# Kernel optimization log

Measured on AMD Instinct MI355X. Metric: run time of the kernel, lower is better.

Reference implementation:

```python
import jax, jax.numpy as jnp
import numpy as np
from jax import lax

SIGMAS = [0.5, 1.0, 2.0]
CHANNELS = 64

def _gaussian_kernel(sigma, channels):
    k = int(6 * sigma + 1) | 1
    x = np.arange(k, dtype=np.float32) - k // 2
    k1 = np.exp(-x ** 2 / (2 * sigma ** 2))
    k2 = np.outer(k1, k1)
    k2 = k2 / k2.sum()
    # depthwise weight layout OIHW with feature_group_count=channels: (C, 1, k, k)
    w = np.broadcast_to(k2[None, None], (channels, 1, k, k)).copy()
    return jnp.asarray(w)

_KERNELS = [_gaussian_kernel(s, CHANNELS) for s in SIGMAS]

def setup_inputs() -> dict:
    key = jax.random.key(0)
    k1, k2, k3 = jax.random.split(key, 3)
    x = jax.random.normal(k1, (8, CHANNELS, 256, 256), dtype=jnp.float32)
    fusion_w = jax.random.normal(k2, (CHANNELS, CHANNELS * len(SIGMAS)), dtype=jnp.float32) * 0.05
    fusion_b = jax.random.normal(k3, (CHANNELS,), dtype=jnp.float32) * 0.05
    return {"x": x, "fusion_w": fusion_w, "fusion_b": fusion_b}

def _depthwise(x, w):
    return lax.conv_general_dilated(
        x, w, window_strides=(1, 1), padding="SAME",
        dimension_numbers=("NCHW", "OIHW", "NCHW"),
        feature_group_count=x.shape[1])

def reference(x, fusion_w, fusion_b):
    # multi-scale depthwise Gaussian blurs, concat on channel dim
    multi_scale = jnp.concatenate([_depthwise(x, w) for w in _KERNELS], axis=1)  # [B, 3C, H, W]
    # 1x1 fusion conv + bias
    fused = jnp.einsum("bchw,oc->bohw", multi_scale, fusion_w) + fusion_b[None, :, None, None]
    return x + fused
```

## Files before the change

### kernel.cpp

```cpp
#include <hip/hip_runtime.h>
#include <hip/hip_bf16.h>
#include <math.h>

#define B_  8
#define C_  64
#define H_  256
#define W_  256
#define HW_ (H_*W_)
#define J_  192
#define TH_ 32

typedef __attribute__((ext_vector_type(8))) short short8;
typedef __attribute__((ext_vector_type(4))) float f32x4;

__device__ __forceinline__ ushort f2bf(float f) {
    union { float f; uint u; } v; v.f = f;
    uint u = v.u;
    return (ushort)((u + 0x7fffu + ((u >> 16) & 1u)) >> 16);
}
__device__ __forceinline__ float bf2f(ushort s) {
    union { uint u; float f; } v; v.u = ((uint)s) << 16;
    return v.f;
}
__device__ __forceinline__ uint pk(float a, float b) {
    return (uint)f2bf(a) | ((uint)f2bf(b) << 16);
}

__global__ __launch_bounds__(256) void k1_mix(
    const float* __restrict__ x, const float* __restrict__ fw,
    ushort* __restrict__ v)
{
    __shared__ ushort lxs[256 * 64];

    const int b      = blockIdx.x >> 8;
    const int pxbase = (blockIdx.x & 255) << 8;
    const int t      = threadIdx.x;
    const int lane   = t & 63;
    const int wv_    = t >> 6;

    {
        const int cg = lane;
        const float* xb = x + (size_t)b * C_ * HW_ + pxbase + 4 * cg;
#pragma unroll
        for (int i = 0; i < 4; ++i) {
            const int cb = wv_ * 4 + i * 16;
            const int c4 = wv_ + i * 4;
            float4 r0 = *(const float4*)(xb + (size_t)(cb + 0) * HW_);
            float4 r1 = *(const float4*)(xb + (size_t)(cb + 1) * HW_);
            float4 r2 = *(const float4*)(xb + (size_t)(cb + 2) * HW_);
            float4 r3 = *(const float4*)(xb + (size_t)(cb + 3) * HW_);
            const int sbase = c4 ^ (cg & 15);
            ushort* dst = &lxs[(4 * cg) * 64];
            *(uint2*)(dst + 0*64 + ((sbase ^ 0) * 4)) = make_uint2(pk(r0.x, r1.x), pk(r2.x, r3.x));
            *(uint2*)(dst + 1*64 + ((sbase ^ 4) * 4)) = make_uint2(pk(r0.y, r1.y), pk(r2.y, r3.y));
            *(uint2*)(dst + 2*64 + ((sbase ^ 8) * 4)) = make_uint2(pk(r0.z, r1.z), pk(r2.z, r3.z));
            *(uint2*)(dst + 3*64 + ((sbase ^ 12) * 4)) = make_uint2(pk(r0.w, r1.w), pk(r2.w, r3.w));
        }
    }

    const int n = lane & 15;
    const int q = lane >> 4;
    union Frag { short8 v; uint u[4]; };
    Frag wf[3][2];
#pragma unroll
    for (int i = 0; i < 3; ++i) {
        const int j  = (wv_ * 3 + i) * 16 + n;
        const float* wr = fw + (size_t)(j & 63) * J_ + (j >> 6) * 64;
#pragma unroll
        for (int kh = 0; kh < 2; ++kh) {
            float4 w0 = *(const float4*)(wr + kh * 32 + q * 8);
            float4 w1 = *(const float4*)(wr + kh * 32 + q * 8 + 4);
            wf[i][kh].u[0] = pk(w0.x, w0.y);
            wf[i][kh].u[1] = pk(w0.z, w0.w);
            wf[i][kh].u[2] = pk(w1.x, w1.y);
            wf[i][kh].u[3] = pk(w1.z, w1.w);
        }
    }

    __syncthreads();

    for (int mt = 0; mt < 16; ++mt) {
        const int px = mt * 16 + (lane & 15);
        const ushort* row = &lxs[px * 64];
        const int s = ((px >> 2) & 15) ^ ((px & 3) << 2);
        Frag a0, a1;
        {
            uint2 lo  = *(const uint2*)&row[((2*q    ) ^ s) * 4];
            uint2 hi  = *(const uint2*)&row[((2*q + 1) ^ s) * 4];
            a0.u[0] = lo.x;  a0.u[1] = lo.y;  a0.u[2] = hi.x;  a0.u[3] = hi.y;
            uint2 lo1 = *(const uint2*)&row[((8 + 2*q    ) ^ s) * 4];
            uint2 hi1 = *(const uint2*)&row[((8 + 2*q + 1) ^ s) * 4];
            a1.u[0] = lo1.x; a1.u[1] = lo1.y; a1.u[2] = hi1.x; a1.u[3] = hi1.y;
        }
#pragma unroll
        for (int i = 0; i < 3; ++i) {
            f32x4 acc = {0.f, 0.f, 0.f, 0.f};
            acc = __builtin_amdgcn_mfma_f32_16x16x32_bf16(a0.v, wf[i][0].v, acc, 0, 0, 0);
            acc = __builtin_amdgcn_mfma_f32_16x16x32_bf16(a1.v, wf[i][1].v, acc, 0, 0, 0);
            const int j   = (wv_ * 3 + i) * 16 + n;
            const int pxg = pxbase + mt * 16 + q * 4;
            *(uint2*)&v[(size_t)(b * J_ + j) * HW_ + pxg] =
                make_uint2(pk(acc[0], acc[1]), pk(acc[2], acc[3]));
        }
    }
}

struct Taps {
    float g0[5];
    float g1[7];
    float g2[13];
};

template<int R, int G>
__device__ __forceinline__ void blur_one(
    const ushort* __restrict__ vplane, const float* __restrict__ g,
    ushort* __restrict__ tmp, int h0, int cg, int rw, float4* acc)
{
    const int NR  = TH_ + 2 * R;
    const int K   = 2 * R + 1;
    const int NG  = 2 * G + 1;
    const int OFF = 4 * G - R;
    const int c0  = cg * 4;

    for (int row = rw; row < NR; row += 4) {
        const int gh = h0 - R + row;
        float o0 = 0.f, o1 = 0.f, o2 = 0.f, o3 = 0.f;
        if (gh >= 0 && gh < H_) {
            const ushort* vr = vplane + (size_t)gh * W_;
            float win[NG * 4];
#pragma unroll
            for (int gi = 0; gi < NG; ++gi) {
                const int gg = cg - G + gi;
                uint2 d = (gg >= 0 && gg < 64) ? *(const uint2*)(vr + gg * 4)
                                               : make_uint2(0u, 0u);
                win[gi*4+0] = bf2f((ushort)(d.x & 0xffffu));
                win[gi*4+1] = bf2f((ushort)(d.x >> 16));
                win[gi*4+2] = bf2f((ushort)(d.y & 0xffffu));
                win[gi*4+3] = bf2f((ushort)(d.y >> 16));
            }
#pragma unroll
            for (int dd = 0; dd < K; ++dd) {
                const float gd = g[dd];
                o0 += gd * win[OFF + dd + 0];
                o1 += gd * win[OFF + dd + 1];
                o2 += gd * win[OFF + dd + 2];
                o3 += gd * win[OFF + dd + 3];
            }
        }
        *(uint2*)&tmp[row * W_ + c0] = make_uint2(pk(o0, o1), pk(o2, o3));
    }
    __syncthreads();

    const int base = rw * 8;
#pragma unroll
    for (int k = 0; k < 8 + 2 * R; ++k) {
        uint2 raw = *(const uint2*)&tmp[(base + k) * W_ + c0];
        const float f0 = bf2f((ushort)(raw.x & 0xffffu));
        const float f1 = bf2f((ushort)(raw.x >> 16));
        const float f2 = bf2f((ushort)(raw.y & 0xffffu));
        const float f3 = bf2f((ushort)(raw.y >> 16));
        const int ilo = (k - 2 * R) > 0 ? (k - 2 * R) : 0;
        const int ihi = k < 7 ? k : 7;
#pragma unroll
        for (int i = ilo; i <= ihi; ++i) {
            const float gd = g[k - i];
            acc[i].x += gd * f0;
            acc[i].y += gd * f1;
            acc[i].z += gd * f2;
            acc[i].w += gd * f3;
        }
    }
    __syncthreads();
}

__global__ __launch_bounds__(256) void k2_blur(
    const ushort* __restrict__ v, const float* __restrict__ x,
    const float* __restrict__ bias, float* __restrict__ out,
    Taps taps)
{
    __shared__ ushort tmp[(TH_ + 12) * W_];

    const int t    = blockIdx.x;
    const int tile = t & 7;
    const int o    = (t >> 3) & 63;
    const int b    = t >> 9;
    const int h0   = tile * TH_;
    const int cg   = threadIdx.x & 63;
    const int rw   = threadIdx.x >> 6;
    const int c0   = cg * 4;

    float4 acc[TH_ / 4];
#pragma unroll
    for (int i = 0; i < TH_ / 4; ++i) acc[i] = make_float4(0.f, 0.f, 0.f, 0.f);

    const ushort* vp = v + (size_t)(b * J_ + o) * HW_;
    blur_one<2, 1>(vp,                       taps.g0, tmp, h0, cg, rw, acc);
    blur_one<3, 1>(vp + (size_t)C_ * HW_,    taps.g1, tmp, h0, cg, rw, acc);
    blur_one<6, 2>(vp + (size_t)(2*C_) * HW_, taps.g2, tmp, h0, cg, rw, acc);

    const float* xp = x   + ((size_t)b * C_ + o) * HW_ + (size_t)h0 * W_;
    float*       op = out + ((size_t)b * C_ + o) * HW_ + (size_t)h0 * W_;
    const float bo = bias[o];
#pragma unroll
    for (int i = 0; i < TH_ / 4; ++i) {
        const int row = rw * 8 + i;
        float4 xv = *(const float4*)&xp[(size_t)row * W_ + c0];
        float4 r;
        r.x = xv.x + bo + acc[i].x;
        r.y = xv.y + bo + acc[i].y;
        r.z = xv.z + bo + acc[i].z;
        r.w = xv.w + bo + acc[i].w;
        *(float4*)&op[(size_t)row * W_ + c0] = r;
    }
}

static void make_taps(Taps& t)
{
    auto fill = [](float* g, int k, double sigma) {
        int r = k / 2;
        double s = 0.0;
        for (int i = 0; i < k; ++i) {
            double w = exp(-(double)((i - r) * (i - r)) / (2.0 * sigma * sigma));
            g[i] = (float)w;
            s += w;
        }
        for (int i = 0; i < k; ++i) g[i] = (float)((double)g[i] / s);
    };
    fill(t.g0, 5, 0.5);
    fill(t.g1, 7, 1.0);
    fill(t.g2, 13, 2.0);
}

extern "C" void kernel_launch(void* const* d_in, const int* in_sizes, int n_in,
                              void* d_out, int out_size, void* d_ws, size_t ws_size,
                              hipStream_t stream)
{
    const float* x  = (const float*)d_in[0];
    const float* fw = (const float*)d_in[1];
    const float* fb = (const float*)d_in[2];
    float* out = (float*)d_out;
    ushort* v = (ushort*)d_ws;
    Taps taps;
    make_taps(taps);

    k1_mix<<<dim3(B_ * (HW_ / 256)), dim3(256), 0, stream>>>(x, fw, v);
    k2_blur<<<dim3(B_ * C_ * (H_ / TH_)), dim3(256), 0, stream>>>(v, x, fb, out, taps);
}
```

Measured before the change: 494.6 us.

## Fuse separable blur passes in registers, drop shared-memory staging and barriers

The blur kernel no longer writes horizontally blurred rows to LDS and syncs before the vertical pass. Each thread now recomputes the horizontal blur for its own 8+2R halo rows from global memory and accumulates the vertical taps directly in registers. This removes the LDS round trip, the bf16 rounding of the intermediate and the block barriers, and launch bounds request higher occupancy. In exchange, halo rows are recomputed and reloaded per wave, adding redundant global reads and ALU work.

```diff
diff --git a/kernel.cpp b/kernel.cpp
--- a/kernel.cpp
+++ b/kernel.cpp
@@ -24,6 +24,12 @@
 }
 __device__ __forceinline__ uint pk(float a, float b) {
     return (uint)f2bf(a) | ((uint)f2bf(b) << 16);
+}
+__device__ __forceinline__ float bflo(uint u) {
+    union { uint u; float f; } v; v.u = u << 16; return v.f;
+}
+__device__ __forceinline__ float bfhi(uint u) {
+    union { uint u; float f; } v; v.u = u & 0xffff0000u; return v.f;
 }
 
 __global__ __launch_bounds__(256) void k1_mix(
@@ -112,19 +118,16 @@
 };
 
 template<int R, int G>
-__device__ __forceinline__ void blur_one(
+__device__ __forceinline__ void blur_scale(
     const ushort* __restrict__ vplane, const float* __restrict__ g,
-    ushort* __restrict__ tmp, int h0, int cg, int rw, float4* acc)
-{
-    const int NR  = TH_ + 2 * R;
-    const int K   = 2 * R + 1;
+    int row0, int cg, float4* acc)
+{
     const int NG  = 2 * G + 1;
     const int OFF = 4 * G - R;
-    const int c0  = cg * 4;
-
-    for (int row = rw; row < NR; row += 4) {
-        const int gh = h0 - R + row;
-        float o0 = 0.f, o1 = 0.f, o2 = 0.f, o3 = 0.f;
+    const int K   = 2 * R + 1;
+#pragma unroll
+    for (int k = 0; k < 8 + 2 * R; ++k) {
+        const int gh = row0 - R + k;
         if (gh >= 0 && gh < H_) {
             const ushort* vr = vplane + (size_t)gh * W_;
             float win[NG * 4];
@@ -133,84 +136,67 @@
                 const int gg = cg - G + gi;
                 uint2 d = (gg >= 0 && gg < 64) ? *(const uint2*)(vr + gg * 4)
                                                : make_uint2(0u, 0u);
-                win[gi*4+0] = bf2f((ushort)(d.x & 0xffffu));
-                win[gi*4+1] = bf2f((ushort)(d.x >> 16));
-                win[gi*4+2] = bf2f((ushort)(d.y & 0xffffu));
-                win[gi*4+3] = bf2f((ushort)(d.y >> 16));
+                win[gi*4+0] = bflo(d.x); win[gi*4+1] = bfhi(d.x);
+                win[gi*4+2] = bflo(d.y); win[gi*4+3] = bfhi(d.y);
             }
+            float t0 = 0.f, t1 = 0.f, t2 = 0.f, t3 = 0.f;
 #pragma unroll
             for (int dd = 0; dd < K; ++dd) {
                 const float gd = g[dd];
-                o0 += gd * win[OFF + dd + 0];
-                o1 += gd * win[OFF + dd + 1];
-                o2 += gd * win[OFF + dd + 2];
-                o3 += gd * win[OFF + dd + 3];
+                t0 += gd * win[OFF + dd + 0];
+                t1 += gd * win[OFF + dd + 1];
+                t2 += gd * win[OFF + dd + 2];
+                t3 += gd * win[OFF + dd + 3];
             }
-        }
-        *(uint2*)&tmp[row * W_ + c0] = make_uint2(pk(o0, o1), pk(o2, o3));
-    }
-    __syncthreads();
-
-    const int base = rw * 8;
-#pragma unroll
-    for (int k = 0; k < 8 + 2 * R; ++k) {
-        uint2 raw = *(const uint2*)&tmp[(base + k) * W_ + c0];
-        const float f0 = bf2f((ushort)(raw.x & 0xffffu));
-        const float f1 = bf2f((ushort)(raw.x >> 16));
-        const float f2 = bf2f((ushort)(raw.y & 0xffffu));
-        const float f3 = bf2f((ushort)(raw.y >> 16));
-        const int ilo = (k - 2 * R) > 0 ? (k - 2 * R) : 0;
-        const int ihi = k < 7 ? k : 7;
-#pragma unroll
-        for (int i = ilo; i <= ihi; ++i) {
-            const float gd = g[k - i];
-            acc[i].x += gd * f0;
-            acc[i].y += gd * f1;
-            acc[i].z += gd * f2;
-            acc[i].w += gd * f3;
-        }
-    }
-    __syncthreads();
-}
-
-__global__ __launch_bounds__(256) void k2_blur(
+            const int ilo = (k - 2 * R) > 0 ? (k - 2 * R) : 0;
+            const int ihi = k < 7 ? k : 7;
+#pragma unroll
+            for (int i = ilo; i <= ihi; ++i) {
+                const float gd = g[k - i];
+                acc[i].x += gd * t0;
+                acc[i].y += gd * t1;
+                acc[i].z += gd * t2;
+                acc[i].w += gd * t3;
+            }
+        }
+    }
+}
+
+__global__ __launch_bounds__(256, 4) void k2_blur(
     const ushort* __restrict__ v, const float* __restrict__ x,
     const float* __restrict__ bias, float* __restrict__ out,
     Taps taps)
 {
-    __shared__ ushort tmp[(TH_ + 12) * W_];
-
     const int t    = blockIdx.x;
     const int tile = t & 7;
     const int o    = (t >> 3) & 63;
     const int b    = t >> 9;
-    const int h0   = tile * TH_;
     const int cg   = threadIdx.x & 63;
     const int rw   = threadIdx.x >> 6;
     const int c0   = cg * 4;
-
-    float4 acc[TH_ / 4];
-#pragma unroll
-    for (int i = 0; i < TH_ / 4; ++i) acc[i] = make_float4(0.f, 0.f, 0.f, 0.f);
+    const int row0 = tile * TH_ + rw * 8;
+
+    float4 acc[8];
+#pragma unroll
+    for (int i = 0; i < 8; ++i) acc[i] = make_float4(0.f, 0.f, 0.f, 0.f);
 
     const ushort* vp = v + (size_t)(b * J_ + o) * HW_;
-    blur_one<2, 1>(vp,                       taps.g0, tmp, h0, cg, rw, acc);
-    blur_one<3, 1>(vp + (size_t)C_ * HW_,    taps.g1, tmp, h0, cg, rw, acc);
-    blur_one<6, 2>(vp + (size_t)(2*C_) * HW_, taps.g2, tmp, h0, cg, rw, acc);
-
-    const float* xp = x   + ((size_t)b * C_ + o) * HW_ + (size_t)h0 * W_;
-    float*       op = out + ((size_t)b * C_ + o) * HW_ + (size_t)h0 * W_;
+    blur_scale<2, 1>(vp,                        taps.g0, row0, cg, acc);
+    blur_scale<3, 1>(vp + (size_t)C_ * HW_,     taps.g1, row0, cg, acc);
+    blur_scale<6, 2>(vp + (size_t)(2*C_) * HW_, taps.g2, row0, cg, acc);
+
+    const float* xp = x   + ((size_t)b * C_ + o) * HW_ + (size_t)row0 * W_;
+    float*       op = out + ((size_t)b * C_ + o) * HW_ + (size_t)row0 * W_;
     const float bo = bias[o];
 #pragma unroll
-    for (int i = 0; i < TH_ / 4; ++i) {
-        const int row = rw * 8 + i;
-        float4 xv = *(const float4*)&xp[(size_t)row * W_ + c0];
+    for (int i = 0; i < 8; ++i) {
+        float4 xv = *(const float4*)&xp[(size_t)i * W_ + c0];
         float4 r;
         r.x = xv.x + bo + acc[i].x;
         r.y = xv.y + bo + acc[i].y;
         r.z = xv.z + bo + acc[i].z;
         r.w = xv.w + bo + acc[i].w;
-        *(float4*)&op[(size_t)row * W_ + c0] = r;
+        *(float4*)&op[(size_t)i * W_ + c0] = r;
     }
 }
 
@@ -240,6 +226,7 @@
     const float* fb = (const float*)d_in[2];
     float* out = (float*)d_out;
     ushort* v = (ushort*)d_ws;
+
     Taps taps;
     make_taps(taps);
 
```

Result: faster. 431.0 us (-12.9%).
